# Kernel tuning notes

Measured on AMD Instinct MI355X. Metric: run time of the kernel, lower is better.

Reference implementation:

```python
import jax, jax.numpy as jnp
import numpy as np

GAMMA = 0.99
LAM = 0.95
CLIP = 0.2
VALUE_COEFF = 0.5
ENTROPY_COEFF = 0.01
T = 500_000
S = 128
A = 16


def _mlp(x, W1, b1, W2, b2, W3, b3):
    h = jax.nn.relu(x @ W1 + b1)
    h = jax.nn.relu(h @ W2 + b2)
    return h @ W3 + b3


def setup_inputs() -> dict:
    key = jax.random.key(0)
    ks = jax.random.split(key, 12)
    states = jax.random.normal(ks[0], (T, S), dtype=jnp.float32)
    next_states = jax.random.normal(ks[1], (T, S), dtype=jnp.float32)
    rewards = jax.random.normal(ks[2], (T,), dtype=jnp.float32)
    dones = (jax.random.uniform(ks[3], (T,)) < 0.01).astype(jnp.float32)
    actions = jax.random.randint(ks[4], (T,), 0, A)
    # old log-probs of taken actions (valid log-probabilities)
    old_logp = jnp.log(jax.random.uniform(ks[5], (T,), minval=1e-3, maxval=1.0))

    def lin(k, fan_in, fan_out):
        lim = 1.0 / np.sqrt(fan_in)
        return jax.random.uniform(k, (fan_in, fan_out), minval=-lim, maxval=lim, dtype=jnp.float32)

    return {
        'states': states, 'next_states': next_states, 'rewards': rewards,
        'dones': dones, 'actions': actions, 'old_logp': old_logp,
        'aW1': lin(ks[6], S, 64), 'ab1': jnp.zeros((64,), jnp.float32),
        'aW2': lin(ks[7], 64, 64), 'ab2': jnp.zeros((64,), jnp.float32),
        'aW3': lin(ks[8], 64, A), 'ab3': jnp.zeros((A,), jnp.float32),
        'cW1': lin(ks[9], S, 64), 'cb1': jnp.zeros((64,), jnp.float32),
        'cW2': lin(ks[10], 64, 64), 'cb2': jnp.zeros((64,), jnp.float32),
        'cW3': lin(ks[11], 64, 1), 'cb3': jnp.zeros((1,), jnp.float32),
    }


def reference(states, next_states, rewards, dones, actions, old_logp,
              aW1, ab1, aW2, ab2, aW3, ab3,
              cW1, cb1, cW2, cb2, cW3, cb3):
    # ---- critic values and TD deltas ----
    values = _mlp(states, cW1, cb1, cW2, cb2, cW3, cb3)[:, 0]        # [T]
    next_values = _mlp(next_states, cW1, cb1, cW2, cb2, cW3, cb3)[:, 0]
    not_done = 1.0 - dones
    deltas = rewards + GAMMA * next_values * not_done - values       # [T]

    # ---- GAE: reverse-time linear recurrence a_t = c_t * a_{t+1} + d_t ----
    coef = GAMMA * LAM * not_done

    def step(carry, cd):
        c, d = cd
        a = c * carry + d
        return a, a

    _, advantages = jax.lax.scan(step, jnp.float32(0.0), (coef, deltas), reverse=True)
    returns = advantages + values
    adv_n = (advantages - advantages.mean()) / (jnp.std(advantages, ddof=1) + 1e-8)

    # ---- actor: clipped surrogate ----
    probs = jax.nn.softmax(_mlp(states, aW1, ab1, aW2, ab2, aW3, ab3), axis=-1)  # [T, A]
    logp = jnp.log(jnp.take_along_axis(probs, actions[:, None], axis=1))[:, 0]   # [T]
    ratios = jnp.exp(logp - old_logp)
    surr1 = ratios * adv_n
    surr2 = jnp.clip(ratios, 1.0 - CLIP, 1.0 + CLIP) * adv_n
    actor_loss = -jnp.minimum(surr1, surr2).mean()

    # ---- critic MSE loss ----
    critic_loss = jnp.mean((values - returns) ** 2)

    # ---- entropy bonus ----
    entropy_loss = jnp.mean(-jnp.sum(probs * jnp.log(probs + 1e-8), axis=-1))

    total_loss = actor_loss + VALUE_COEFF * critic_loss - ENTROPY_COEFF * entropy_loss
    return jnp.stack([total_loss, actor_loss, critic_loss, entropy_loss])
```

## Files before the change

### kernel.cpp

```cpp
#include <hip/hip_runtime.h>
#include <hip/hip_bf16.h>

#define T_N 500000
#define NTILE 31250
#define NBLK 1024
#define NWAVES NBLK
#define NCHUNK 4096
#define CHUNKL 128
#define NPART 1024

typedef __attribute__((ext_vector_type(8))) short short8v;
typedef __attribute__((ext_vector_type(4))) float float4v;

__device__ __forceinline__ short f2bf(float f) {
    __hip_bfloat16 b = __float2bfloat16(f);
    return *reinterpret_cast<short*>(&b);
}
__device__ __forceinline__ float bf2f(short s) {
    return __uint_as_float(((unsigned)(unsigned short)s) << 16);
}

__device__ __forceinline__ short8v cvt8(const float4 a, const float4 b) {
    short8v r;
    r[0] = f2bf(a.x); r[1] = f2bf(a.y); r[2] = f2bf(a.z); r[3] = f2bf(a.w);
    r[4] = f2bf(b.x); r[5] = f2bf(b.y); r[6] = f2bf(b.z); r[7] = f2bf(b.w);
    return r;
}

#define FC1 0
#define FA1 16
#define FC2 32
#define FA2 40
#define FA3 48
#define NFRAG 50

__device__ __forceinline__ int featperm(int c, int r) {
    return ((c >> 1) << 5) + ((r >> 2) << 3) + ((c & 1) << 2) + (r & 3);
}

__global__ __launch_bounds__(64) void k_pack(
    const float* __restrict__ cW1, const float* __restrict__ aW1,
    const float* __restrict__ cW2, const float* __restrict__ aW2,
    const float* __restrict__ aW3, short8v* __restrict__ packed)
{
    const int f = blockIdx.x, l = threadIdx.x;
    const int g = l >> 4, r = l & 15;
    const float* W; int s, c, ncol; bool perm = true;
    if (f < FA1)      { W = cW1; s = f >> 2;         c = f & 3;         ncol = 64; }
    else if (f < FC2) { W = aW1; s = (f - FA1) >> 2; c = (f - FA1) & 3; ncol = 64; }
    else if (f < FA2) { W = cW2; s = (f - FC2) >> 2; c = (f - FC2) & 3; ncol = 64; }
    else if (f < FA3) { W = aW2; s = (f - FA2) >> 2; c = (f - FA2) & 3; ncol = 64; }
    else              { W = aW3; s = f - FA3;        c = 0;             ncol = 16; perm = false; }
    const int col = perm ? featperm(c, r) : r;
    short8v frag;
    #pragma unroll
    for (int j = 0; j < 8; ++j) {
        int k = s * 32 + g * 8 + j;
        frag[j] = f2bf(W[k * ncol + col]);
    }
    packed[f * 64 + l] = frag;
}

__device__ __forceinline__ void mk_bfrag(const float4v* acc, short8v* bf) {
    #pragma unroll
    for (int s = 0; s < 2; ++s)
        #pragma unroll
        for (int j = 0; j < 8; ++j)
            bf[s][j] = f2bf(fmaxf(acc[2 * s + (j >> 2)][j & 3], 0.f));
}

__global__ __launch_bounds__(64) void k_mlp(
    const float* __restrict__ states, const float* __restrict__ next_states,
    const short8v* __restrict__ pk,
    const float* __restrict__ cb1, const float* __restrict__ ab1,
    const float* __restrict__ cb2, const float* __restrict__ ab2,
    const float* __restrict__ ab3,
    const float* __restrict__ cW3, const float* __restrict__ cb3,
    float* __restrict__ v_o, float* __restrict__ nv_o,
    short* __restrict__ logit_o)
{
    const int l = threadIdx.x;
    const int g = l >> 4, q = l & 15;
    const int wid = blockIdx.x;
    const float cb3v = cb3[0];
    int off[4];
    #pragma unroll
    for (int c = 0; c < 4; ++c) off[c] = ((c >> 1) << 5) + (g << 3) + ((c & 1) << 2);

    short8v wf[NFRAG];
    #pragma unroll
    for (int f = 0; f < NFRAG; ++f) wf[f] = pk[f * 64 + l];

    float4 bc1v[4], bc2v[4], ba1v[4], ba2v[4], w3v[4];
    #pragma unroll
    for (int c = 0; c < 4; ++c) {
        bc1v[c] = *reinterpret_cast<const float4*>(cb1 + off[c]);
        bc2v[c] = *reinterpret_cast<const float4*>(cb2 + off[c]);
        ba1v[c] = *reinterpret_cast<const float4*>(ab1 + off[c]);
        ba2v[c] = *reinterpret_cast<const float4*>(ab2 + off[c]);
        w3v[c]  = *reinterpret_cast<const float4*>(cW3 + off[c]);
    }
    float4 ab3v = *reinterpret_cast<const float4*>(ab3 + g * 4);

    float4 ra[8], rb[8];
    {
        const float* xs = states + ((long long)wid * 16 + q) * 128 + g * 8;
        const float* xn = next_states + ((long long)wid * 16 + q) * 128 + g * 8;
        #pragma unroll
        for (int s = 0; s < 4; ++s) {
            ra[2 * s]     = *reinterpret_cast<const float4*>(xs + s * 32);
            ra[2 * s + 1] = *reinterpret_cast<const float4*>(xs + s * 32 + 4);
            rb[2 * s]     = *reinterpret_cast<const float4*>(xn + s * 32);
            rb[2 * s + 1] = *reinterpret_cast<const float4*>(xn + s * 32 + 4);
        }
    }

    for (long long t = wid; t < NTILE; t += NWAVES) {
        const long long r0 = t * 16;

        short8v sa[4], na[4];
        #pragma unroll
        for (int s = 0; s < 4; ++s) {
            sa[s] = cvt8(ra[2 * s], ra[2 * s + 1]);
            na[s] = cvt8(rb[2 * s], rb[2 * s + 1]);
        }

        if (t + NWAVES < NTILE) {
            const float* xs = states + ((t + NWAVES) * 16 + q) * 128 + g * 8;
            const float* xn = next_states + ((t + NWAVES) * 16 + q) * 128 + g * 8;
            #pragma unroll
            for (int s = 0; s < 4; ++s) {
                ra[2 * s]     = *reinterpret_cast<const float4*>(xs + s * 32);
                ra[2 * s + 1] = *reinterpret_cast<const float4*>(xs + s * 32 + 4);
                rb[2 * s]     = *reinterpret_cast<const float4*>(xn + s * 32);
                rb[2 * s + 1] = *reinterpret_cast<const float4*>(xn + s * 32 + 4);
            }
        }

        float4v accC[4], accN[4];
        #pragma unroll
        for (int c = 0; c < 4; ++c) {
            accC[c] = (float4v){bc1v[c].x, bc1v[c].y, bc1v[c].z, bc1v[c].w};
            accN[c] = accC[c];
        }
        #pragma unroll
        for (int s = 0; s < 4; ++s)
            #pragma unroll
            for (int c = 0; c < 4; ++c) {
                accC[c] = __builtin_amdgcn_mfma_f32_16x16x32_bf16(wf[FC1 + s * 4 + c], sa[s], accC[c], 0, 0, 0);
                accN[c] = __builtin_amdgcn_mfma_f32_16x16x32_bf16(wf[FC1 + s * 4 + c], na[s], accN[c], 0, 0, 0);
            }
        short8v bC[2], bN[2];
        mk_bfrag(accC, bC);
        mk_bfrag(accN, bN);

        float4v c2C[4], c2N[4];
        #pragma unroll
        for (int c = 0; c < 4; ++c) {
            c2C[c] = (float4v){bc2v[c].x, bc2v[c].y, bc2v[c].z, bc2v[c].w};
            c2N[c] = c2C[c];
        }
        #pragma unroll
        for (int s = 0; s < 2; ++s)
            #pragma unroll
            for (int c = 0; c < 4; ++c) {
                c2C[c] = __builtin_amdgcn_mfma_f32_16x16x32_bf16(wf[FC2 + s * 4 + c], bC[s], c2C[c], 0, 0, 0);
                c2N[c] = __builtin_amdgcn_mfma_f32_16x16x32_bf16(wf[FC2 + s * 4 + c], bN[s], c2N[c], 0, 0, 0);
            }

        float vp = 0.f, np = 0.f;
        #pragma unroll
        for (int c = 0; c < 4; ++c) {
            const float wv4[4] = {w3v[c].x, w3v[c].y, w3v[c].z, w3v[c].w};
            #pragma unroll
            for (int u = 0; u < 4; ++u) {
                vp = fmaf(fmaxf(c2C[c][u], 0.f), wv4[u], vp);
                np = fmaf(fmaxf(c2N[c][u], 0.f), wv4[u], np);
            }
        }
        vp += __shfl_xor(vp, 16); vp += __shfl_xor(vp, 32);
        np += __shfl_xor(np, 16); np += __shfl_xor(np, 32);
        if (g == 0) {
            v_o[r0 + q]  = vp + cb3v;
            nv_o[r0 + q] = np + cb3v;
        }

        float4v aA[4];
        #pragma unroll
        for (int c = 0; c < 4; ++c)
            aA[c] = (float4v){ba1v[c].x, ba1v[c].y, ba1v[c].z, ba1v[c].w};
        #pragma unroll
        for (int s = 0; s < 4; ++s)
            #pragma unroll
            for (int c = 0; c < 4; ++c)
                aA[c] = __builtin_amdgcn_mfma_f32_16x16x32_bf16(wf[FA1 + s * 4 + c], sa[s], aA[c], 0, 0, 0);
        short8v bA[2];
        mk_bfrag(aA, bA);

        float4v a2[4];
        #pragma unroll
        for (int c = 0; c < 4; ++c)
            a2[c] = (float4v){ba2v[c].x, ba2v[c].y, ba2v[c].z, ba2v[c].w};
        #pragma unroll
        for (int s = 0; s < 2; ++s)
            #pragma unroll
            for (int c = 0; c < 4; ++c)
                a2[c] = __builtin_amdgcn_mfma_f32_16x16x32_bf16(wf[FA2 + s * 4 + c], bA[s], a2[c], 0, 0, 0);
        short8v b3[2];
        mk_bfrag(a2, b3);

        float4v a3 = (float4v){ab3v.x, ab3v.y, ab3v.z, ab3v.w};
        #pragma unroll
        for (int s = 0; s < 2; ++s)
            a3 = __builtin_amdgcn_mfma_f32_16x16x32_bf16(wf[FA3 + s], b3[s], a3, 0, 0, 0);

        unsigned w0 = ((unsigned)(unsigned short)f2bf(a3[1]) << 16) |
                      (unsigned)(unsigned short)f2bf(a3[0]);
        unsigned w1 = ((unsigned)(unsigned short)f2bf(a3[3]) << 16) |
                      (unsigned)(unsigned short)f2bf(a3[2]);
        uint2 lw; lw.x = w0; lw.y = w1;
        *reinterpret_cast<uint2*>(logit_o + (r0 + q) * 16 + g * 4) = lw;
    }
}

__device__ __forceinline__ void dc_elem(float v, float nv, float rw, float dn,
                                        float& d, float& c) {
    float nd = 1.f - dn;
    d = fmaf(0.99f * nd, nv, rw) - v;
    c = (0.99f * 0.95f) * nd;
}

__global__ __launch_bounds__(256) void k_gae_chunk(
    const float* __restrict__ v_i, const float* __restrict__ nv_i,
    const float* __restrict__ rewards, const float* __restrict__ dones,
    float* __restrict__ P, float* __restrict__ Q)
{
    const int c = blockIdx.x * 256 + threadIdx.x;
    const long long lo = (long long)c * CHUNKL;
    float p = 1.f, a = 0.f;
    if (lo < T_N) {
        const int n = (int)((T_N - lo < CHUNKL) ? (T_N - lo) : CHUNKL);
        for (int j = (n >> 2) - 1; j >= 0; --j) {
            float4 vv = *reinterpret_cast<const float4*>(&v_i[lo + 4 * j]);
            float4 nn = *reinterpret_cast<const float4*>(&nv_i[lo + 4 * j]);
            float4 rw = *reinterpret_cast<const float4*>(&rewards[lo + 4 * j]);
            float4 dn = *reinterpret_cast<const float4*>(&dones[lo + 4 * j]);
            float d0, c0, d1, c1, d2, c2, d3, c3;
            dc_elem(vv.x, nn.x, rw.x, dn.x, d0, c0);
            dc_elem(vv.y, nn.y, rw.y, dn.y, d1, c1);
            dc_elem(vv.z, nn.z, rw.z, dn.z, d2, c2);
            dc_elem(vv.w, nn.w, rw.w, dn.w, d3, c3);
            a = fmaf(c3, a, d3);
            a = fmaf(c2, a, d2);
            a = fmaf(c1, a, d1);
            a = fmaf(c0, a, d0);
            p *= c0 * c1 * c2 * c3;
        }
    }
    P[c] = p; Q[c] = a;
}

__global__ __launch_bounds__(1024) void k_gae_scan(
    const float* __restrict__ P, const float* __restrict__ Q,
    float* __restrict__ carry)
{
    __shared__ float sp[1024], sq[1024];
    const int t = threadIdx.x, b = t * 4;
    float p = P[b + 3], q = Q[b + 3];
    #pragma unroll
    for (int c = 2; c >= 0; --c) {
        float pc = P[b + c], qc = Q[b + c];
        q = fmaf(pc, q, qc);
        p = pc * p;
    }
    sp[t] = p; sq[t] = q;
    __syncthreads();
    for (int d = 1; d < 1024; d <<= 1) {
        float pp = sp[t], qq = sq[t];
        float p2 = 1.f, q2 = 0.f;
        const bool has = (t + d) < 1024;
        if (has) { p2 = sp[t + d]; q2 = sq[t + d]; }
        __syncthreads();
        if (has) { sp[t] = pp * p2; sq[t] = fmaf(pp, q2, qq); }
        __syncthreads();
    }
    float x = (t + 1 < 1024) ? sq[t + 1] : 0.f;
    #pragma unroll
    for (int c = 3; c >= 0; --c) {
        carry[b + c] = x;
        x = fmaf(P[b + c], x, Q[b + c]);
    }
}

__global__ __launch_bounds__(256) void k_gae_apply(
    const float* __restrict__ v_i, const float* __restrict__ nv_i,
    const float* __restrict__ rewards, const float* __restrict__ dones,
    const float* __restrict__ carry, float* __restrict__ adv,
    float* __restrict__ part)
{
    const int c = blockIdx.x * 256 + threadIdx.x;
    const long long lo = (long long)c * CHUNKL;
    float s = 0.f, s2 = 0.f;
    if (lo < T_N) {
        const int n = (int)((T_N - lo < CHUNKL) ? (T_N - lo) : CHUNKL);
        float a = carry[c];
        for (int j = (n >> 2) - 1; j >= 0; --j) {
            float4 vv = *reinterpret_cast<const float4*>(&v_i[lo + 4 * j]);
            float4 nn = *reinterpret_cast<const float4*>(&nv_i[lo + 4 * j]);
            float4 rw = *reinterpret_cast<const float4*>(&rewards[lo + 4 * j]);
            float4 dn = *reinterpret_cast<const float4*>(&dones[lo + 4 * j]);
            float d0, c0, d1, c1, d2, c2, d3, c3;
            dc_elem(vv.x, nn.x, rw.x, dn.x, d0, c0);
            dc_elem(vv.y, nn.y, rw.y, dn.y, d1, c1);
            dc_elem(vv.z, nn.z, rw.z, dn.z, d2, c2);
            dc_elem(vv.w, nn.w, rw.w, dn.w, d3, c3);
            float a3 = fmaf(c3, a, d3);
            float a2v = fmaf(c2, a3, d2);
            float a1 = fmaf(c1, a2v, d1);
            float a0 = fmaf(c0, a1, d0);
            float4 o; o.x = a0; o.y = a1; o.z = a2v; o.w = a3;
            *reinterpret_cast<float4*>(&adv[lo + 4 * j]) = o;
            a = a0;
            s += a0 + a1 + a2v + a3;
            s2 += a0 * a0 + a1 * a1 + a2v * a2v + a3 * a3;
        }
    }
    #pragma unroll
    for (int o = 32; o > 0; o >>= 1) { s += __shfl_down(s, o); s2 += __shfl_down(s2, o); }
    __shared__ float l0[4], l1[4];
    const int wv = threadIdx.x >> 6, ln = threadIdx.x & 63;
    if (ln == 0) { l0[wv] = s; l1[wv] = s2; }
    __syncthreads();
    if (threadIdx.x == 0) {
        part[blockIdx.x * 2]     = l0[0] + l0[1] + l0[2] + l0[3];
        part[blockIdx.x * 2 + 1] = l1[0] + l1[1] + l1[2] + l1[3];
    }
}

__global__ __launch_bounds__(256) void k_actor(
    const float* __restrict__ adv, const short* __restrict__ logits,
    const float* __restrict__ old_logp, const int* __restrict__ actions,
    const float* __restrict__ part, float* __restrict__ part4)
{
    __shared__ float st[2];
    if (threadIdx.x == 0) {
        float S = 0.f, S2 = 0.f;
        #pragma unroll
        for (int i = 0; i < 16; ++i) { S += part[2 * i]; S2 += part[2 * i + 1]; }
        const float Tf = (float)T_N;
        float mean = S / Tf;
        float var = (S2 - S * S / Tf) / (Tf - 1.f);
        st[0] = mean;
        st[1] = 1.f / (sqrtf(fmaxf(var, 0.f)) + 1e-8f);
    }
    __syncthreads();
    const float mean = st[0], isd = st[1];
    float sm = 0.f, sent = 0.f;
    for (long long i = (long long)blockIdx.x * 256 + threadIdx.x; i < T_N;
         i += (long long)gridDim.x * 256) {
        const short8v* lp = reinterpret_cast<const short8v*>(logits) + i * 2;
        short8v lo0 = lp[0], lo1 = lp[1];
        float lg[16];
        #pragma unroll
        for (int j = 0; j < 8; ++j) { lg[j] = bf2f(lo0[j]); lg[8 + j] = bf2f(lo1[j]); }
        float m = lg[0];
        #pragma unroll
        for (int a = 1; a < 16; ++a) m = fmaxf(m, lg[a]);
        float se = 0.f, tt = 0.f;
        #pragma unroll
        for (int a = 0; a < 16; ++a) {
            float e = __expf(lg[a] - m);
            se += e;
            tt = fmaf(e, lg[a], tt);
        }
        float ls = __logf(se);
        float ent = m + ls - tt / se;
        const int act = actions[i];
        float lsel = lg[0];
        #pragma unroll
        for (int a = 1; a < 16; ++a) lsel = (a == act) ? lg[a] : lsel;
        float logp = lsel - m - ls;
        float rt = __expf(logp - old_logp[i]);
        float an = (adv[i] - mean) * isd;
        sm += fminf(rt * an, fminf(fmaxf(rt, 0.8f), 1.2f) * an);
        sent += ent;
    }
    #pragma unroll
    for (int o = 32; o > 0; o >>= 1) { sm += __shfl_down(sm, o); sent += __shfl_down(sent, o); }
    __shared__ float l0[4], l1[4];
    const int wv = threadIdx.x >> 6, ln = threadIdx.x & 63;
    if (ln == 0) { l0[wv] = sm; l1[wv] = sent; }
    __syncthreads();
    if (threadIdx.x == 0) {
        part4[blockIdx.x * 2]     = l0[0] + l0[1] + l0[2] + l0[3];
        part4[blockIdx.x * 2 + 1] = l1[0] + l1[1] + l1[2] + l1[3];
    }
}

__global__ __launch_bounds__(1024) void k_final(
    const float* __restrict__ part4, const float* __restrict__ part,
    float* __restrict__ out)
{
    const int t = threadIdx.x;
    float sm = part4[t * 2], se = part4[t * 2 + 1];
    #pragma unroll
    for (int o = 32; o > 0; o >>= 1) { sm += __shfl_down(sm, o); se += __shfl_down(se, o); }
    __shared__ float l0[16], l1[16];
    const int wv = t >> 6, ln = t & 63;
    if (ln == 0) { l0[wv] = sm; l1[wv] = se; }
    __syncthreads();
    if (t == 0) {
        float SM = 0.f, SE = 0.f;
        #pragma unroll
        for (int i = 0; i < 16; ++i) { SM += l0[i]; SE += l1[i]; }
        float S2 = 0.f;
        #pragma unroll
        for (int i = 0; i < 16; ++i) S2 += part[2 * i + 1];
        const float Tf = (float)T_N;
        float actor_loss = -SM / Tf;
        float ent_loss = SE / Tf;
        float critic_loss = S2 / Tf;
        float total = actor_loss + 0.5f * critic_loss - 0.01f * ent_loss;
        out[0] = total; out[1] = actor_loss; out[2] = critic_loss; out[3] = ent_loss;
    }
}

extern "C" void kernel_launch(void* const* d_in, const int* in_sizes, int n_in,
                              void* d_out, int out_size, void* d_ws, size_t ws_size,
                              hipStream_t stream) {
    (void)in_sizes; (void)n_in; (void)out_size; (void)ws_size;
    const float* states      = (const float*)d_in[0];
    const float* next_states = (const float*)d_in[1];
    const float* rewards     = (const float*)d_in[2];
    const float* dones       = (const float*)d_in[3];
    const int*   actions     = (const int*)d_in[4];
    const float* old_logp    = (const float*)d_in[5];
    const float* aW1 = (const float*)d_in[6];  const float* ab1 = (const float*)d_in[7];
    const float* aW2 = (const float*)d_in[8];  const float* ab2 = (const float*)d_in[9];
    const float* aW3 = (const float*)d_in[10]; const float* ab3 = (const float*)d_in[11];
    const float* cW1 = (const float*)d_in[12]; const float* cb1 = (const float*)d_in[13];
    const float* cW2 = (const float*)d_in[14]; const float* cb2 = (const float*)d_in[15];
    const float* cW3 = (const float*)d_in[16]; const float* cb3 = (const float*)d_in[17];
    float* out = (float*)d_out;

    short* logits = (short*)d_ws;
    float* fbase = (float*)(logits + (size_t)T_N * 16);
    float* v_ws  = fbase;
    float* nv_ws = fbase + (size_t)T_N;
    float* adv   = fbase + 2 * (size_t)T_N;
    float* P     = fbase + 3 * (size_t)T_N;
    float* Q     = P + NCHUNK;
    float* carry = Q + NCHUNK;
    float* part  = carry + NCHUNK;
    float* part4 = part + 32;
    short8v* packed = (short8v*)(part4 + 2048);

    k_pack<<<NFRAG, 64, 0, stream>>>(cW1, aW1, cW2, aW2, aW3, packed);
    k_mlp<<<NBLK, 64, 0, stream>>>(
        states, next_states, packed,
        cb1, ab1, cb2, ab2, ab3, cW3, cb3, v_ws, nv_ws, logits);
    k_gae_chunk<<<NCHUNK / 256, 256, 0, stream>>>(v_ws, nv_ws, rewards, dones, P, Q);
    k_gae_scan<<<1, 1024, 0, stream>>>(P, Q, carry);
    k_gae_apply<<<NCHUNK / 256, 256, 0, stream>>>(v_ws, nv_ws, rewards, dones, carry, adv, part);
    k_actor<<<NPART, 256, 0, stream>>>(adv, logits, old_logp, actions, part, part4);
    k_final<<<1, 1024, 0, stream>>>(part4, part, out);
}
```

Baseline: 193.2 us.

## Serialize critic/actor passes and stagger next_states prefetch to cut register pressure

Restructures the MLP tile loop so the states pass (critic, then actor) runs first and the next_states critic pass runs afterwards, reusing a single accumulator set instead of interleaved C/N accumulators. The prefetch of next_states rows for the following tile is moved to just before its consumption, which spreads the loads across the loop body. Launch bounds now request one wave per EU minimum. The aim is lower register pressure and more staggered memory traffic, at the cost of less MFMA independence, since the states and next_states chains no longer interleave.

Measured after the change: 184.9 us (median of 2 runs). 1.05x faster.

```diff
diff --git a/kernel.cpp b/kernel.cpp
--- a/kernel.cpp
+++ b/kernel.cpp
@@ -69,7 +69,7 @@
             bf[s][j] = f2bf(fmaxf(acc[2 * s + (j >> 2)][j & 3], 0.f));
 }
 
-__global__ __launch_bounds__(64) void k_mlp(
+__global__ __launch_bounds__(64, 1) void k_mlp(
     const float* __restrict__ states, const float* __restrict__ next_states,
     const short8v* __restrict__ pk,
     const float* __restrict__ cb1, const float* __restrict__ ab1,
@@ -100,7 +100,7 @@
         ba2v[c] = *reinterpret_cast<const float4*>(ab2 + off[c]);
         w3v[c]  = *reinterpret_cast<const float4*>(cW3 + off[c]);
     }
-    float4 ab3v = *reinterpret_cast<const float4*>(ab3 + g * 4);
+    const float4 ab3v = *reinterpret_cast<const float4*>(ab3 + g * 4);
 
     float4 ra[8], rb[8];
     {
@@ -117,109 +117,129 @@
 
     for (long long t = wid; t < NTILE; t += NWAVES) {
         const long long r0 = t * 16;
-
-        short8v sa[4], na[4];
-        #pragma unroll
-        for (int s = 0; s < 4; ++s) {
-            sa[s] = cvt8(ra[2 * s], ra[2 * s + 1]);
-            na[s] = cvt8(rb[2 * s], rb[2 * s + 1]);
-        }
-
-        if (t + NWAVES < NTILE) {
+        const bool more = (t + NWAVES) < NTILE;
+
+        short8v sa[4];
+        #pragma unroll
+        for (int s = 0; s < 4; ++s) sa[s] = cvt8(ra[2 * s], ra[2 * s + 1]);
+        if (more) {
             const float* xs = states + ((t + NWAVES) * 16 + q) * 128 + g * 8;
-            const float* xn = next_states + ((t + NWAVES) * 16 + q) * 128 + g * 8;
             #pragma unroll
             for (int s = 0; s < 4; ++s) {
                 ra[2 * s]     = *reinterpret_cast<const float4*>(xs + s * 32);
                 ra[2 * s + 1] = *reinterpret_cast<const float4*>(xs + s * 32 + 4);
+            }
+        }
+
+        float4v acc[4];
+        short8v bf[2];
+
+        #pragma unroll
+        for (int c = 0; c < 4; ++c)
+            acc[c] = (float4v){bc1v[c].x, bc1v[c].y, bc1v[c].z, bc1v[c].w};
+        #pragma unroll
+        for (int s = 0; s < 4; ++s)
+            #pragma unroll
+            for (int c = 0; c < 4; ++c)
+                acc[c] = __builtin_amdgcn_mfma_f32_16x16x32_bf16(wf[FC1 + s * 4 + c], sa[s], acc[c], 0, 0, 0);
+        mk_bfrag(acc, bf);
+
+        #pragma unroll
+        for (int c = 0; c < 4; ++c)
+            acc[c] = (float4v){bc2v[c].x, bc2v[c].y, bc2v[c].z, bc2v[c].w};
+        #pragma unroll
+        for (int s = 0; s < 2; ++s)
+            #pragma unroll
+            for (int c = 0; c < 4; ++c)
+                acc[c] = __builtin_amdgcn_mfma_f32_16x16x32_bf16(wf[FC2 + s * 4 + c], bf[s], acc[c], 0, 0, 0);
+
+        {
+            float vp = 0.f;
+            #pragma unroll
+            for (int c = 0; c < 4; ++c) {
+                const float w4[4] = {w3v[c].x, w3v[c].y, w3v[c].z, w3v[c].w};
+                #pragma unroll
+                for (int u = 0; u < 4; ++u)
+                    vp = fmaf(fmaxf(acc[c][u], 0.f), w4[u], vp);
+            }
+            vp += __shfl_xor(vp, 16); vp += __shfl_xor(vp, 32);
+            if (g == 0) v_o[r0 + q] = vp + cb3v;
+        }
+
+        #pragma unroll
+        for (int c = 0; c < 4; ++c)
+            acc[c] = (float4v){ba1v[c].x, ba1v[c].y, ba1v[c].z, ba1v[c].w};
+        #pragma unroll
+        for (int s = 0; s < 4; ++s)
+            #pragma unroll
+            for (int c = 0; c < 4; ++c)
+                acc[c] = __builtin_amdgcn_mfma_f32_16x16x32_bf16(wf[FA1 + s * 4 + c], sa[s], acc[c], 0, 0, 0);
+        mk_bfrag(acc, bf);
+
+        #pragma unroll
+        for (int c = 0; c < 4; ++c)
+            acc[c] = (float4v){ba2v[c].x, ba2v[c].y, ba2v[c].z, ba2v[c].w};
+        #pragma unroll
+        for (int s = 0; s < 2; ++s)
+            #pragma unroll
+            for (int c = 0; c < 4; ++c)
+                acc[c] = __builtin_amdgcn_mfma_f32_16x16x32_bf16(wf[FA2 + s * 4 + c], bf[s], acc[c], 0, 0, 0);
+        mk_bfrag(acc, bf);
+
+        {
+            float4v a3 = (float4v){ab3v.x, ab3v.y, ab3v.z, ab3v.w};
+            #pragma unroll
+            for (int s = 0; s < 2; ++s)
+                a3 = __builtin_amdgcn_mfma_f32_16x16x32_bf16(wf[FA3 + s], bf[s], a3, 0, 0, 0);
+            unsigned w0 = ((unsigned)(unsigned short)f2bf(a3[1]) << 16) |
+                          (unsigned)(unsigned short)f2bf(a3[0]);
+            unsigned w1 = ((unsigned)(unsigned short)f2bf(a3[3]) << 16) |
+                          (unsigned)(unsigned short)f2bf(a3[2]);
+            uint2 lw; lw.x = w0; lw.y = w1;
+            *reinterpret_cast<uint2*>(logit_o + (r0 + q) * 16 + g * 4) = lw;
+        }
+
+        short8v na[4];
+        #pragma unroll
+        for (int s = 0; s < 4; ++s) na[s] = cvt8(rb[2 * s], rb[2 * s + 1]);
+        if (more) {
+            const float* xn = next_states + ((t + NWAVES) * 16 + q) * 128 + g * 8;
+            #pragma unroll
+            for (int s = 0; s < 4; ++s) {
                 rb[2 * s]     = *reinterpret_cast<const float4*>(xn + s * 32);
                 rb[2 * s + 1] = *reinterpret_cast<const float4*>(xn + s * 32 + 4);
             }
         }
 
-        float4v accC[4], accN[4];
-        #pragma unroll
-        for (int c = 0; c < 4; ++c) {
-            accC[c] = (float4v){bc1v[c].x, bc1v[c].y, bc1v[c].z, bc1v[c].w};
-            accN[c] = accC[c];
-        }
+        #pragma unroll
+        for (int c = 0; c < 4; ++c)
+            acc[c] = (float4v){bc1v[c].x, bc1v[c].y, bc1v[c].z, bc1v[c].w};
         #pragma unroll
         for (int s = 0; s < 4; ++s)
             #pragma unroll
+            for (int c = 0; c < 4; ++c)
+                acc[c] = __builtin_amdgcn_mfma_f32_16x16x32_bf16(wf[FC1 + s * 4 + c], na[s], acc[c], 0, 0, 0);
+        mk_bfrag(acc, bf);
+        #pragma unroll
+        for (int c = 0; c < 4; ++c)
+            acc[c] = (float4v){bc2v[c].x, bc2v[c].y, bc2v[c].z, bc2v[c].w};
+        #pragma unroll
+        for (int s = 0; s < 2; ++s)
+            #pragma unroll
+            for (int c = 0; c < 4; ++c)
+                acc[c] = __builtin_amdgcn_mfma_f32_16x16x32_bf16(wf[FC2 + s * 4 + c], bf[s], acc[c], 0, 0, 0);
+        {
+            float np = 0.f;
+            #pragma unroll
             for (int c = 0; c < 4; ++c) {
-                accC[c] = __builtin_amdgcn_mfma_f32_16x16x32_bf16(wf[FC1 + s * 4 + c], sa[s], accC[c], 0, 0, 0);
-                accN[c] = __builtin_amdgcn_mfma_f32_16x16x32_bf16(wf[FC1 + s * 4 + c], na[s], accN[c], 0, 0, 0);
+                const float w4[4] = {w3v[c].x, w3v[c].y, w3v[c].z, w3v[c].w};
+                #pragma unroll
+                for (int u = 0; u < 4; ++u)
+                    np = fmaf(fmaxf(acc[c][u], 0.f), w4[u], np);
             }
-        short8v bC[2], bN[2];
-        mk_bfrag(accC, bC);
-        mk_bfrag(accN, bN);
-
-        float4v c2C[4], c2N[4];
-        #pragma unroll
-        for (int c = 0; c < 4; ++c) {
-            c2C[c] = (float4v){bc2v[c].x, bc2v[c].y, bc2v[c].z, bc2v[c].w};
-            c2N[c] = c2C[c];
-        }
-        #pragma unroll
-        for (int s = 0; s < 2; ++s)
-            #pragma unroll
-            for (int c = 0; c < 4; ++c) {
-                c2C[c] = __builtin_amdgcn_mfma_f32_16x16x32_bf16(wf[FC2 + s * 4 + c], bC[s], c2C[c], 0, 0, 0);
-                c2N[c] = __builtin_amdgcn_mfma_f32_16x16x32_bf16(wf[FC2 + s * 4 + c], bN[s], c2N[c], 0, 0, 0);
-            }
-
-        float vp = 0.f, np = 0.f;
-        #pragma unroll
-        for (int c = 0; c < 4; ++c) {
-            const float wv4[4] = {w3v[c].x, w3v[c].y, w3v[c].z, w3v[c].w};
-            #pragma unroll
-            for (int u = 0; u < 4; ++u) {
-                vp = fmaf(fmaxf(c2C[c][u], 0.f), wv4[u], vp);
-                np = fmaf(fmaxf(c2N[c][u], 0.f), wv4[u], np);
-            }
-        }
-        vp += __shfl_xor(vp, 16); vp += __shfl_xor(vp, 32);
-        np += __shfl_xor(np, 16); np += __shfl_xor(np, 32);
-        if (g == 0) {
-            v_o[r0 + q]  = vp + cb3v;
-            nv_o[r0 + q] = np + cb3v;
-        }
-
-        float4v aA[4];
-        #pragma unroll
-        for (int c = 0; c < 4; ++c)
-            aA[c] = (float4v){ba1v[c].x, ba1v[c].y, ba1v[c].z, ba1v[c].w};
-        #pragma unroll
-        for (int s = 0; s < 4; ++s)
-            #pragma unroll
-            for (int c = 0; c < 4; ++c)
-                aA[c] = __builtin_amdgcn_mfma_f32_16x16x32_bf16(wf[FA1 + s * 4 + c], sa[s], aA[c], 0, 0, 0);
-        short8v bA[2];
-        mk_bfrag(aA, bA);
-
-        float4v a2[4];
-        #pragma unroll
-        for (int c = 0; c < 4; ++c)
-            a2[c] = (float4v){ba2v[c].x, ba2v[c].y, ba2v[c].z, ba2v[c].w};
-        #pragma unroll
-        for (int s = 0; s < 2; ++s)
-            #pragma unroll
-            for (int c = 0; c < 4; ++c)
-                a2[c] = __builtin_amdgcn_mfma_f32_16x16x32_bf16(wf[FA2 + s * 4 + c], bA[s], a2[c], 0, 0, 0);
-        short8v b3[2];
-        mk_bfrag(a2, b3);
-
-        float4v a3 = (float4v){ab3v.x, ab3v.y, ab3v.z, ab3v.w};
-        #pragma unroll
-        for (int s = 0; s < 2; ++s)
-            a3 = __builtin_amdgcn_mfma_f32_16x16x32_bf16(wf[FA3 + s], b3[s], a3, 0, 0, 0);
-
-        unsigned w0 = ((unsigned)(unsigned short)f2bf(a3[1]) << 16) |
-                      (unsigned)(unsigned short)f2bf(a3[0]);
-        unsigned w1 = ((unsigned)(unsigned short)f2bf(a3[3]) << 16) |
-                      (unsigned)(unsigned short)f2bf(a3[2]);
-        uint2 lw; lw.x = w0; lw.y = w1;
-        *reinterpret_cast<uint2*>(logit_o + (r0 + q) * 16 + g * 4) = lw;
+            np += __shfl_xor(np, 16); np += __shfl_xor(np, 32);
+            if (g == 0) nv_o[r0 + q] = np + cb3v;
+        }
     }
 }
 
```
